# Kernel tuning notes

Hardware: AMD Instinct MI355X
Metric: run time of the kernel (lower is better)

Reference implementation:

```python
import jax, jax.numpy as jnp
import numpy as np

N_NODES = 50000
N_EDGES = 800000
IN_DIM = 128
HIDDEN = 64
HEADS = 4
N_GRAPHS = 256
NEG_SLOPE = 0.2  # PyG GATConv default


def gat_conv(x, src, dst, W, a_src, a_dst, b):
    """PyG-style GATConv (concat=True), eval mode (no dropout).
    x: [N, F_in]; src/dst: [E] (self-loops already included);
    W: [H*C, F_in]; a_src/a_dst: [H, C]; b: [H*C].
    """
    N = x.shape[0]
    H, C = a_src.shape
    h = (x @ W.T).reshape(N, H, C)                      # [N, H, C]
    alo = (h * a_src[None]).sum(-1)                     # [N, H]
    ahi = (h * a_dst[None]).sum(-1)                     # [N, H]
    e = jax.nn.leaky_relu(alo[src] + ahi[dst], NEG_SLOPE)  # [E, H]
    # segment softmax over destination neighborhoods
    m = jax.ops.segment_max(e, dst, num_segments=N)     # [N, H]
    ex = jnp.exp(e - m[dst])
    denom = jax.ops.segment_sum(ex, dst, num_segments=N)
    alpha = ex / (denom[dst] + 1e-16)                   # [E, H]
    out = jax.ops.segment_sum(h[src] * alpha[:, :, None], dst, num_segments=N)
    return out.reshape(N, H * C) + b


def setup_inputs() -> dict:
    key = jax.random.key(0)
    ks = jax.random.split(key, 24)
    p = lambda k, s: (jax.random.normal(k, s, jnp.float32) * 0.1)
    x = jax.random.normal(ks[0], (N_NODES, IN_DIM), jnp.float32)
    edge_index = jax.random.randint(ks[1], (2, N_EDGES), 0, N_NODES, jnp.int64 if jax.config.jax_enable_x64 else jnp.int32)
    batch_idx = jnp.sort(jax.random.randint(ks[2], (N_NODES,), 0, N_GRAPHS))
    HC = HIDDEN * HEADS
    return {
        "x": x, "edge_index": edge_index, "batch_idx": batch_idx,
        "W1": p(ks[3], (HC, IN_DIM)), "as1": p(ks[4], (HEADS, HIDDEN)), "ad1": p(ks[5], (HEADS, HIDDEN)), "b1": jnp.zeros((HC,), jnp.float32),
        "W2": p(ks[6], (HC, HC)), "as2": p(ks[7], (HEADS, HIDDEN)), "ad2": p(ks[8], (HEADS, HIDDEN)), "b2": jnp.zeros((HC,), jnp.float32),
        "W3": p(ks[9], (HIDDEN, HC)), "as3": p(ks[10], (1, HIDDEN)), "ad3": p(ks[11], (1, HIDDEN)), "b3": jnp.zeros((HIDDEN,), jnp.float32),
        "Wc1": p(ks[12], (HIDDEN, HIDDEN)), "bc1": jnp.zeros((HIDDEN,), jnp.float32),
        "Wc2": p(ks[13], (1, HIDDEN)), "bc2": jnp.zeros((1,), jnp.float32),
        "Wr1": p(ks[14], (HIDDEN, HIDDEN)), "br1": jnp.zeros((HIDDEN,), jnp.float32),
        "Wr2": p(ks[15], (1, HIDDEN)), "br2": jnp.zeros((1,), jnp.float32),
    }


def reference(x, edge_index, batch_idx, W1, as1, ad1, b1, W2, as2, ad2, b2, W3, as3, ad3, b3, Wc1, bc1, Wc2, bc2, Wr1, br1, Wr2, br2):
    N = x.shape[0]
    loops = jnp.arange(N, dtype=edge_index.dtype)
    src = jnp.concatenate([edge_index[0], loops])  # add_self_loops=True (PyG default)
    dst = jnp.concatenate([edge_index[1], loops])
    h = jax.nn.elu(gat_conv(x, src, dst, W1, as1, ad1, b1))
    h = jax.nn.elu(gat_conv(h, src, dst, W2, as2, ad2, b2))
    h = jax.nn.elu(gat_conv(h, src, dst, W3, as3, ad3, b3))  # [N, HIDDEN]
    # global mean pool over graphs
    cnt = jax.ops.segment_sum(jnp.ones((N,), h.dtype), batch_idx, num_segments=N_GRAPHS)
    g = jax.ops.segment_sum(h, batch_idx, num_segments=N_GRAPHS) / jnp.maximum(cnt, 1.0)[:, None]
    cls_logit = (jax.nn.relu(g @ Wc1.T + bc1) @ Wc2.T + bc2).reshape(-1)
    reg_pred = (jax.nn.relu(g @ Wr1.T + br1) @ Wr2.T + br2).reshape(-1)
    return (cls_logit, reg_pred)
```

## Files before the change

kernel.cpp:

```cpp
#include <hip/hip_runtime.h>

#define N_NODES 50000
#define N_EDGES 800000
#define EP_EDGES (N_EDGES + N_NODES)
#define N_GRAPHS 256
#define NBLK_SCAN ((N_NODES + 255) / 256)
#define POOL_CHUNK ((N_NODES + 255) / 256)

typedef unsigned short u16;
typedef __attribute__((ext_vector_type(8))) short s8v;
typedef __attribute__((ext_vector_type(4))) float f4v;

__device__ __forceinline__ u16 fb(float f) {
  unsigned u = __float_as_uint(f);
  return (u16)((u + 0x7fffu + ((u >> 16) & 1u)) >> 16);
}
__device__ __forceinline__ float bfl(unsigned p) {
  return __uint_as_float(p << 16);
}
__device__ __forceinline__ float bfh(unsigned p) {
  return __uint_as_float(p & 0xffff0000u);
}
__device__ __forceinline__ float bff(u16 s) {
  return __uint_as_float(((unsigned)s) << 16);
}

#define W_N1 32768
#define W_N2 (W_N1 + 65536)
#define W_N3 (W_N2 + 16384)
__global__ void f2bw(const float* __restrict__ w1, const float* __restrict__ w2,
                     const float* __restrict__ w3, u16* __restrict__ w1b,
                     u16* __restrict__ w2b, u16* __restrict__ w3b) {
  int i = blockIdx.x * 256 + threadIdx.x;
  if (i < W_N1) w1b[i] = fb(w1[i]);
  else if (i < W_N2) w2b[i - W_N1] = fb(w2[i - W_N1]);
  else if (i < W_N3) w3b[i - W_N2] = fb(w3[i - W_N2]);
}

__device__ __forceinline__ void score_epilogue(
    f4v (&acc)[4][4], const float* __restrict__ a_src,
    const float* __restrict__ a_dst, float* __restrict__ alo,
    float* __restrict__ ahi, int m0, int n0, int wi, int wj, int quad, int fr,
    int M) {
  const int head = (n0 + wj) >> 6;
  float as[4], ad[4];
#pragma unroll
  for (int j = 0; j < 4; ++j) {
    int col = n0 + wj + j * 16 + fr;
    as[j] = a_src[col];
    ad[j] = a_dst[col];
  }
#pragma unroll
  for (int i = 0; i < 4; ++i) {
#pragma unroll
    for (int r = 0; r < 4; ++r) {
      float s = 0.f, d = 0.f;
#pragma unroll
      for (int j = 0; j < 4; ++j) {
        s += acc[i][j][r] * as[j];
        d += acc[i][j][r] * ad[j];
      }
#pragma unroll
      for (int off = 8; off; off >>= 1) {
        s += __shfl_xor(s, off, 64);
        d += __shfl_xor(d, off, 64);
      }
      int row = m0 + wi + i * 16 + quad * 4 + r;
      if (fr == 0 && row < M) {
        alo[row * 4 + head] = s;
        ahi[row * 4 + head] = d;
      }
    }
  }
}

__global__ __launch_bounds__(256) void gemm128(
    const u16* __restrict__ A, const u16* __restrict__ W,
    u16* __restrict__ C, const float* __restrict__ a_src,
    const float* __restrict__ a_dst, float* __restrict__ alo,
    float* __restrict__ ahi, int M, int Nout, int K) {
  __shared__ u16 As[128][40];
  __shared__ u16 Bs[128][40];
  const int t = threadIdx.x;
  const int m0 = blockIdx.y * 128, n0 = blockIdx.x * 128;
  const int rq = t >> 2, q = t & 3;
  const int w = t >> 6, lane = t & 63;
  const int wi = (w & 1) * 64, wj = (w >> 1) * 64;
  const int quad = lane >> 4, fr = lane & 15;

  f4v acc[4][4] = {};
  for (int k0 = 0; k0 < K; k0 += 32) {
    uint4 av[2], bv[2];
#pragma unroll
    for (int g = 0; g < 2; ++g) {
      int r = rq + g * 64;
      int m = m0 + r;
      av[g] = (m < M) ? *(const uint4*)&A[(size_t)m * K + k0 + q * 8]
                      : make_uint4(0, 0, 0, 0);
      bv[g] = *(const uint4*)&W[(size_t)(n0 + r) * K + k0 + q * 8];
    }
    __syncthreads();
#pragma unroll
    for (int g = 0; g < 2; ++g) {
      *(uint4*)&As[rq + g * 64][q * 8] = av[g];
      *(uint4*)&Bs[rq + g * 64][q * 8] = bv[g];
    }
    __syncthreads();
    s8v af[4], bf_[4];
#pragma unroll
    for (int i = 0; i < 4; ++i) {
      af[i] = *(const s8v*)&As[wi + i * 16 + fr][quad * 8];
      bf_[i] = *(const s8v*)&Bs[wj + i * 16 + fr][quad * 8];
    }
#pragma unroll
    for (int i = 0; i < 4; ++i)
#pragma unroll
      for (int j = 0; j < 4; ++j)
        acc[i][j] =
            __builtin_amdgcn_mfma_f32_16x16x32_bf16(af[i], bf_[j], acc[i][j], 0, 0, 0);
  }
#pragma unroll
  for (int i = 0; i < 4; ++i) {
    int rbase = m0 + wi + i * 16 + quad * 4;
#pragma unroll
    for (int j = 0; j < 4; ++j) {
      int col = n0 + wj + j * 16 + fr;
#pragma unroll
      for (int r = 0; r < 4; ++r) {
        int row = rbase + r;
        if (row < M) C[(size_t)row * Nout + col] = fb(acc[i][j][r]);
      }
    }
  }
  score_epilogue(acc, a_src, a_dst, alo, ahi, m0, n0, wi, wj, quad, fr, M);
}

__global__ __launch_bounds__(256) void gemm128_f32(
    const float* __restrict__ A, const u16* __restrict__ W,
    u16* __restrict__ C, const float* __restrict__ a_src,
    const float* __restrict__ a_dst, float* __restrict__ alo,
    float* __restrict__ ahi, int M, int Nout, int K) {
  __shared__ u16 As[128][40];
  __shared__ u16 Bs[128][40];
  const int t = threadIdx.x;
  const int m0 = blockIdx.y * 128, n0 = blockIdx.x * 128;
  const int rq = t >> 2, q = t & 3;
  const int w = t >> 6, lane = t & 63;
  const int wi = (w & 1) * 64, wj = (w >> 1) * 64;
  const int quad = lane >> 4, fr = lane & 15;

  f4v acc[4][4] = {};
  for (int k0 = 0; k0 < K; k0 += 32) {
    uint4 av[2], bv[2];
#pragma unroll
    for (int g = 0; g < 2; ++g) {
      int r = rq + g * 64;
      int m = m0 + r;
      if (m < M) {
        float4 f0 = *(const float4*)&A[(size_t)m * K + k0 + q * 8];
        float4 f1 = *(const float4*)&A[(size_t)m * K + k0 + q * 8 + 4];
        av[g].x = (unsigned)fb(f0.x) | ((unsigned)fb(f0.y) << 16);
        av[g].y = (unsigned)fb(f0.z) | ((unsigned)fb(f0.w) << 16);
        av[g].z = (unsigned)fb(f1.x) | ((unsigned)fb(f1.y) << 16);
        av[g].w = (unsigned)fb(f1.z) | ((unsigned)fb(f1.w) << 16);
      } else {
        av[g] = make_uint4(0, 0, 0, 0);
      }
      bv[g] = *(const uint4*)&W[(size_t)(n0 + r) * K + k0 + q * 8];
    }
    __syncthreads();
#pragma unroll
    for (int g = 0; g < 2; ++g) {
      *(uint4*)&As[rq + g * 64][q * 8] = av[g];
      *(uint4*)&Bs[rq + g * 64][q * 8] = bv[g];
    }
    __syncthreads();
    s8v af[4], bf_[4];
#pragma unroll
    for (int i = 0; i < 4; ++i) {
      af[i] = *(const s8v*)&As[wi + i * 16 + fr][quad * 8];
      bf_[i] = *(const s8v*)&Bs[wj + i * 16 + fr][quad * 8];
    }
#pragma unroll
    for (int i = 0; i < 4; ++i)
#pragma unroll
      for (int j = 0; j < 4; ++j)
        acc[i][j] =
            __builtin_amdgcn_mfma_f32_16x16x32_bf16(af[i], bf_[j], acc[i][j], 0, 0, 0);
  }
#pragma unroll
  for (int i = 0; i < 4; ++i) {
    int rbase = m0 + wi + i * 16 + quad * 4;
#pragma unroll
    for (int j = 0; j < 4; ++j) {
      int col = n0 + wj + j * 16 + fr;
#pragma unroll
      for (int r = 0; r < 4; ++r) {
        int row = rbase + r;
        if (row < M) C[(size_t)row * Nout + col] = fb(acc[i][j][r]);
      }
    }
  }
  score_epilogue(acc, a_src, a_dst, alo, ahi, m0, n0, wi, wj, quad, fr, M);
}

__global__ __launch_bounds__(256) void gemm_bf16(
    const u16* __restrict__ A, const u16* __restrict__ W,
    u16* __restrict__ C, int M, int Nout, int K) {
  __shared__ u16 As[64][40];
  __shared__ u16 Bs[64][40];
  const int t = threadIdx.x;
  const int m0 = blockIdx.y * 64, n0 = blockIdx.x * 64;
  const int r = t >> 2, c = t & 3;
  const int w = t >> 6, lane = t & 63;
  const int mi = (w & 1) * 32, ni = (w >> 1) * 32;
  const int quad = lane >> 4, fr = lane & 15;

  f4v c00{}, c01{}, c10{}, c11{};
  for (int k0 = 0; k0 < K; k0 += 32) {
    uint4 av = make_uint4(0, 0, 0, 0);
    int m = m0 + r;
    if (m < M) av = *(const uint4*)&A[(size_t)m * K + k0 + c * 8];
    uint4 bv = *(const uint4*)&W[(size_t)(n0 + r) * K + k0 + c * 8];
    __syncthreads();
    *(uint4*)&As[r][c * 8] = av;
    *(uint4*)&Bs[r][c * 8] = bv;
    __syncthreads();
    s8v a0 = *(const s8v*)&As[mi + fr][quad * 8];
    s8v a1 = *(const s8v*)&As[mi + 16 + fr][quad * 8];
    s8v b0 = *(const s8v*)&Bs[ni + fr][quad * 8];
    s8v b1 = *(const s8v*)&Bs[ni + 16 + fr][quad * 8];
    c00 = __builtin_amdgcn_mfma_f32_16x16x32_bf16(a0, b0, c00, 0, 0, 0);
    c01 = __builtin_amdgcn_mfma_f32_16x16x32_bf16(a0, b1, c01, 0, 0, 0);
    c10 = __builtin_amdgcn_mfma_f32_16x16x32_bf16(a1, b0, c10, 0, 0, 0);
    c11 = __builtin_amdgcn_mfma_f32_16x16x32_bf16(a1, b1, c11, 0, 0, 0);
  }
  const int col = n0 + ni + fr;
#pragma unroll
  for (int i = 0; i < 4; ++i) {
    int row = m0 + mi + quad * 4 + i;
    if (row < M) {
      C[(size_t)row * Nout + col] = fb(c00[i]);
      C[(size_t)row * Nout + col + 16] = fb(c01[i]);
    }
    int row2 = row + 16;
    if (row2 < M) {
      C[(size_t)row2 * Nout + col] = fb(c10[i]);
      C[(size_t)row2 * Nout + col + 16] = fb(c11[i]);
    }
  }
}

__global__ void k_hist(const int* __restrict__ ei, int* __restrict__ deg) {
  int e = blockIdx.x * 256 + threadIdx.x;
  if (e >= EP_EDGES) return;
  int d = (e < N_EDGES) ? ei[N_EDGES + e] : e - N_EDGES;
  atomicAdd(&deg[d], 1);
}

__global__ void k_scan_local(const int* __restrict__ deg,
                             int* __restrict__ rowstart,
                             int* __restrict__ bsum) {
  __shared__ int sh[256];
  const int tid = threadIdx.x;
  const int i = blockIdx.x * 256 + tid;
  int v = (i < N_NODES) ? deg[i] : 0;
  sh[tid] = v;
  __syncthreads();
  for (int off = 1; off < 256; off <<= 1) {
    int add = (tid >= off) ? sh[tid - off] : 0;
    __syncthreads();
    sh[tid] += add;
    __syncthreads();
  }
  if (i < N_NODES) rowstart[i] = sh[tid] - v;
  if (tid == 255) bsum[blockIdx.x] = sh[255];
}

__global__ void k_scan_bsum(int* __restrict__ bsum, int* __restrict__ boff) {
  __shared__ int sh[256];
  const int tid = threadIdx.x;
  int v = (tid < NBLK_SCAN) ? bsum[tid] : 0;
  sh[tid] = v;
  __syncthreads();
  for (int off = 1; off < 256; off <<= 1) {
    int add = (tid >= off) ? sh[tid - off] : 0;
    __syncthreads();
    sh[tid] += add;
    __syncthreads();
  }
  boff[tid] = sh[tid] - v;
}

__global__ void k_scan_add(int* __restrict__ rowstart,
                           const int* __restrict__ boff) {
  int i = blockIdx.x * 256 + threadIdx.x;
  if (i < N_NODES) rowstart[i] += boff[i >> 8];
  if (i == N_NODES) rowstart[N_NODES] = EP_EDGES;
}

__global__ void k_scatter(const int* __restrict__ ei,
                          const int* __restrict__ rowstart,
                          int* __restrict__ fill, int* __restrict__ esrc) {
  int e = blockIdx.x * 256 + threadIdx.x;
  if (e >= EP_EDGES) return;
  int s, d;
  if (e < N_EDGES) { s = ei[e]; d = ei[N_EDGES + e]; }
  else             { s = d = e - N_EDGES; }
  int pos = rowstart[d] + atomicAdd(&fill[d], 1);
  esrc[pos] = s;
}

__global__ __launch_bounds__(256) void attn_scores1(
    const u16* __restrict__ h, const float* __restrict__ a_src,
    const float* __restrict__ a_dst, float* __restrict__ alo,
    float* __restrict__ ahi) {
  const int t = threadIdx.x;
  const int n = blockIdx.x * 4 + (t >> 6);
  const int lane = t & 63;
  float v = bff(h[(size_t)n * 64 + lane]);
  float s = v * a_src[lane];
  float d = v * a_dst[lane];
#pragma unroll
  for (int off = 32; off; off >>= 1) {
    s += __shfl_xor(s, off, 64);
    d += __shfl_xor(d, off, 64);
  }
  if (lane == 0) {
    alo[n] = s;
    ahi[n] = d;
  }
}

__global__ __launch_bounds__(64) void agg3_4(
    const int* __restrict__ rowstart, const int* __restrict__ esrc,
    const u16* __restrict__ hbuf, const float* __restrict__ alo,
    const float* __restrict__ ahi, const float* __restrict__ bias,
    u16* __restrict__ feat) {
  const int d = blockIdx.x;
  const int lane = threadIdx.x;
  const int head = lane >> 4;
  const int l16 = lane & 15;
  const int c = lane * 4;
  const int s0 = rowstart[d], s1 = rowstart[d + 1];
  const float ah = ahi[d * 4 + head];

  float sm = 0.f;
  for (int j = s0 + l16; j < s1; j += 16) {
    int s = esrc[j];
    float e = alo[s * 4 + head] + ah;
    e = e > 0.f ? e : 0.2f * e;
    sm += __expf(e);
  }
#pragma unroll
  for (int off = 8; off; off >>= 1) sm += __shfl_xor(sm, off, 64);
  const float linv = 1.f / (sm + 1e-16f);

  float o0 = 0.f, o1 = 0.f, o2 = 0.f, o3 = 0.f;
  for (int j = s0; j < s1; j += 8) {
    int ss[8];
    float wq[8];
#pragma unroll
    for (int q = 0; q < 8; ++q) {
      int jj = j + q;
      int sv = esrc[jj < EP_EDGES ? jj : EP_EDGES - 1];
      ss[q] = (jj < s1) ? sv : d;
    }
#pragma unroll
    for (int q = 0; q < 8; ++q) {
      float e = alo[ss[q] * 4 + head] + ah;
      e = e > 0.f ? e : 0.2f * e;
      wq[q] = (j + q < s1) ? __expf(e) * linv : 0.f;
    }
    uint2 hv[8];
#pragma unroll
    for (int q = 0; q < 8; ++q)
      hv[q] = *(const uint2*)&hbuf[(size_t)ss[q] * 256 + c];
#pragma unroll
    for (int q = 0; q < 8; ++q) {
      o0 += wq[q] * bfl(hv[q].x);
      o1 += wq[q] * bfh(hv[q].x);
      o2 += wq[q] * bfl(hv[q].y);
      o3 += wq[q] * bfh(hv[q].y);
    }
  }
  float4 bv = *(const float4*)&bias[c];
  float v0 = o0 + bv.x, v1 = o1 + bv.y, v2 = o2 + bv.z, v3 = o3 + bv.w;
  v0 = v0 > 0.f ? v0 : __expf(v0) - 1.f;
  v1 = v1 > 0.f ? v1 : __expf(v1) - 1.f;
  v2 = v2 > 0.f ? v2 : __expf(v2) - 1.f;
  v3 = v3 > 0.f ? v3 : __expf(v3) - 1.f;
  uint2 pv;
  pv.x = (unsigned)fb(v0) | ((unsigned)fb(v1) << 16);
  pv.y = (unsigned)fb(v2) | ((unsigned)fb(v3) << 16);
  *(uint2*)&feat[(size_t)d * 256 + c] = pv;
}

__global__ __launch_bounds__(64) void agg3_1(
    const int* __restrict__ rowstart, const int* __restrict__ esrc,
    const u16* __restrict__ hbuf, const float* __restrict__ alo,
    const float* __restrict__ ahi, const float* __restrict__ bias,
    float* __restrict__ feat) {
  const int d = blockIdx.x;
  const int t = threadIdx.x;
  const int s0 = rowstart[d], s1 = rowstart[d + 1];
  const float ah = ahi[d];

  float sm = 0.f;
  for (int j = s0 + t; j < s1; j += 64) {
    int s = esrc[j];
    float e = alo[s] + ah;
    e = e > 0.f ? e : 0.2f * e;
    sm += __expf(e);
  }
#pragma unroll
  for (int off = 32; off; off >>= 1) sm += __shfl_xor(sm, off, 64);
  const float linv = 1.f / (sm + 1e-16f);

  float o = 0.f;
  for (int j = s0; j < s1; j += 8) {
    int ss[8];
    float wq[8];
#pragma unroll
    for (int q = 0; q < 8; ++q) {
      int jj = j + q;
      int sv = esrc[jj < EP_EDGES ? jj : EP_EDGES - 1];
      ss[q] = (jj < s1) ? sv : d;
    }
#pragma unroll
    for (int q = 0; q < 8; ++q) {
      float e = alo[ss[q]] + ah;
      e = e > 0.f ? e : 0.2f * e;
      wq[q] = (j + q < s1) ? __expf(e) * linv : 0.f;
    }
    u16 hv[8];
#pragma unroll
    for (int q = 0; q < 8; ++q) hv[q] = hbuf[(size_t)ss[q] * 64 + t];
#pragma unroll
    for (int q = 0; q < 8; ++q) o += wq[q] * bff(hv[q]);
  }
  float v = o + bias[t];
  feat[(size_t)d * 64 + t] = v > 0.f ? v : __expf(v) - 1.f;
}

__global__ __launch_bounds__(64) void pool_seg(
    const float* __restrict__ feat, const int* __restrict__ batch,
    float* __restrict__ gsum, float* __restrict__ gcnt) {
  const int b = blockIdx.x;
  const int t = threadIdx.x;
  int n0 = b * POOL_CHUNK;
  int n1 = n0 + POOL_CHUNK;
  if (n1 > N_NODES) n1 = N_NODES;
  if (n0 >= n1) return;
  int g = batch[n0];
  float acc = 0.f;
  int cnt = 0;
  for (int n = n0; n < n1; ++n) {
    int gn = batch[n];
    if (gn != g) {
      atomicAdd(&gsum[g * 64 + t], acc);
      if (t == 0) atomicAdd(&gcnt[g], (float)cnt);
      acc = 0.f; cnt = 0; g = gn;
    }
    acc += feat[(size_t)n * 64 + t];
    ++cnt;
  }
  atomicAdd(&gsum[g * 64 + t], acc);
  if (t == 0) atomicAdd(&gcnt[g], (float)cnt);
}

__global__ void heads(const float* __restrict__ gsum,
                      const float* __restrict__ gcnt,
                      const float* __restrict__ Wc1, const float* __restrict__ bc1,
                      const float* __restrict__ Wc2, const float* __restrict__ bc2,
                      const float* __restrict__ Wr1, const float* __restrict__ br1,
                      const float* __restrict__ Wr2, const float* __restrict__ br2,
                      float* __restrict__ out) {
  __shared__ float g[64];
  const int gi = blockIdx.x, j = threadIdx.x;
  float cnt = gcnt[gi];
  cnt = cnt < 1.f ? 1.f : cnt;
  g[j] = gsum[gi * 64 + j] / cnt;
  __syncthreads();
  float hc = bc1[j], hr = br1[j];
#pragma unroll 8
  for (int c = 0; c < 64; ++c) {
    float gv = g[c];
    hc += gv * Wc1[j * 64 + c];
    hr += gv * Wr1[j * 64 + c];
  }
  hc = fmaxf(hc, 0.f) * Wc2[j];
  hr = fmaxf(hr, 0.f) * Wr2[j];
#pragma unroll
  for (int off = 32; off; off >>= 1) {
    hc += __shfl_down(hc, off, 64);
    hr += __shfl_down(hr, off, 64);
  }
  if (j == 0) {
    out[gi] = hc + bc2[0];
    out[N_GRAPHS + gi] = hr + br2[0];
  }
}

extern "C" void kernel_launch(void* const* d_in, const int* in_sizes, int n_in,
                              void* d_out, int out_size, void* d_ws,
                              size_t ws_size, hipStream_t stream) {
  const float* x   = (const float*)d_in[0];
  const int* ei    = (const int*)d_in[1];
  const int* batch = (const int*)d_in[2];
  const float* W1  = (const float*)d_in[3];
  const float* as1 = (const float*)d_in[4];
  const float* ad1 = (const float*)d_in[5];
  const float* b1  = (const float*)d_in[6];
  const float* W2  = (const float*)d_in[7];
  const float* as2 = (const float*)d_in[8];
  const float* ad2 = (const float*)d_in[9];
  const float* b2  = (const float*)d_in[10];
  const float* W3  = (const float*)d_in[11];
  const float* as3 = (const float*)d_in[12];
  const float* ad3 = (const float*)d_in[13];
  const float* b3  = (const float*)d_in[14];
  const float* Wc1 = (const float*)d_in[15];
  const float* bc1 = (const float*)d_in[16];
  const float* Wc2 = (const float*)d_in[17];
  const float* bc2 = (const float*)d_in[18];
  const float* Wr1 = (const float*)d_in[19];
  const float* br1 = (const float*)d_in[20];
  const float* Wr2 = (const float*)d_in[21];
  const float* br2 = (const float*)d_in[22];
  float* out = (float*)d_out;

  float* ws = (float*)d_ws;
  u16* h_buf = (u16*)ws;
  float* p = ws + (size_t)N_NODES * 128;
  u16* featb = (u16*)p;
  p += (size_t)N_NODES * 128;
  u16* W1b = (u16*)p; p += 16384;
  u16* W2b = (u16*)p; p += 32768;
  u16* W3b = (u16*)p; p += 8192;
  float* feat3 = p;   p += (size_t)N_NODES * 64;
  float* alo   = p;   p += (size_t)N_NODES * 4;
  float* ahi   = p;   p += (size_t)N_NODES * 4;
  int* rowstart = (int*)p; p += (N_NODES + 4);
  int* esrc    = (int*)p;  p += EP_EDGES;
  float* gsum  = p;   p += N_GRAPHS * 64;
  float* gcnt  = p;
  int* deg  = (int*)alo;
  int* fill = (int*)alo + N_NODES;
  int* bsum = (int*)gsum;
  int* boff = (int*)gsum + 256;

  hipMemsetAsync(deg, 0, (size_t)2 * N_NODES * 4, stream);
  const int eblk = (EP_EDGES + 255) / 256;
  k_hist<<<eblk, 256, 0, stream>>>(ei, deg);
  k_scan_local<<<NBLK_SCAN, 256, 0, stream>>>(deg, rowstart, bsum);
  k_scan_bsum<<<1, 256, 0, stream>>>(bsum, boff);
  k_scan_add<<<(N_NODES + 256) / 256, 256, 0, stream>>>(rowstart, boff);
  k_scatter<<<eblk, 256, 0, stream>>>(ei, rowstart, fill, esrc);

  f2bw<<<(W_N3 + 255) / 256, 256, 0, stream>>>(W1, W2, W3, W1b, W2b, W3b);

  const int MB128 = (N_NODES + 127) / 128;
  const int MB64 = (N_NODES + 63) / 64;
  gemm128_f32<<<dim3(2, MB128), 256, 0, stream>>>(x, W1b, h_buf, as1, ad1, alo,
                                                  ahi, N_NODES, 256, 128);
  agg3_4<<<N_NODES, 64, 0, stream>>>(rowstart, esrc, h_buf, alo, ahi, b1,
                                     featb);
  gemm128<<<dim3(2, MB128), 256, 0, stream>>>(featb, W2b, h_buf, as2, ad2, alo,
                                              ahi, N_NODES, 256, 256);
  agg3_4<<<N_NODES, 64, 0, stream>>>(rowstart, esrc, h_buf, alo, ahi, b2,
                                     featb);
  gemm_bf16<<<dim3(1, MB64), 256, 0, stream>>>(featb, W3b, h_buf, N_NODES, 64, 256);
  attn_scores1<<<N_NODES / 4, 256, 0, stream>>>(h_buf, as3, ad3, alo, ahi);
  agg3_1<<<N_NODES, 64, 0, stream>>>(rowstart, esrc, h_buf, alo, ahi, b3,
                                     feat3);

  hipMemsetAsync(gsum, 0, (size_t)(N_GRAPHS * 64 + N_GRAPHS) * 4, stream);
  pool_seg<<<N_GRAPHS, 64, 0, stream>>>(feat3, batch, gsum, gcnt);
  heads<<<N_GRAPHS, 64, 0, stream>>>(gsum, gcnt, Wc1, bc1, Wc2, bc2, Wr1, br1,
                                     Wr2, br2, out);
}
```

Before: 558.7 us.

## Fuse softmax denominator into aggregation and merge pooling with MLP heads

```diff
diff --git a/kernel.cpp b/kernel.cpp
--- a/kernel.cpp
+++ b/kernel.cpp
@@ -5,7 +5,6 @@
 #define EP_EDGES (N_EDGES + N_NODES)
 #define N_GRAPHS 256
 #define NBLK_SCAN ((N_NODES + 255) / 256)
-#define POOL_CHUNK ((N_NODES + 255) / 256)
 
 typedef unsigned short u16;
 typedef __attribute__((ext_vector_type(8))) short s8v;
@@ -311,28 +310,7 @@
   esrc[pos] = s;
 }
 
-__global__ __launch_bounds__(256) void attn_scores1(
-    const u16* __restrict__ h, const float* __restrict__ a_src,
-    const float* __restrict__ a_dst, float* __restrict__ alo,
-    float* __restrict__ ahi) {
-  const int t = threadIdx.x;
-  const int n = blockIdx.x * 4 + (t >> 6);
-  const int lane = t & 63;
-  float v = bff(h[(size_t)n * 64 + lane]);
-  float s = v * a_src[lane];
-  float d = v * a_dst[lane];
-#pragma unroll
-  for (int off = 32; off; off >>= 1) {
-    s += __shfl_xor(s, off, 64);
-    d += __shfl_xor(d, off, 64);
-  }
-  if (lane == 0) {
-    alo[n] = s;
-    ahi[n] = d;
-  }
-}
-
-__global__ __launch_bounds__(64) void agg3_4(
+__global__ __launch_bounds__(64) void agg4(
     const int* __restrict__ rowstart, const int* __restrict__ esrc,
     const u16* __restrict__ hbuf, const float* __restrict__ alo,
     const float* __restrict__ ahi, const float* __restrict__ bias,
@@ -340,23 +318,11 @@
   const int d = blockIdx.x;
   const int lane = threadIdx.x;
   const int head = lane >> 4;
-  const int l16 = lane & 15;
   const int c = lane * 4;
   const int s0 = rowstart[d], s1 = rowstart[d + 1];
   const float ah = ahi[d * 4 + head];
 
-  float sm = 0.f;
-  for (int j = s0 + l16; j < s1; j += 16) {
-    int s = esrc[j];
-    float e = alo[s * 4 + head] + ah;
-    e = e > 0.f ? e : 0.2f * e;
-    sm += __expf(e);
-  }
-#pragma unroll
-  for (int off = 8; off; off >>= 1) sm += __shfl_xor(sm, off, 64);
-  const float linv = 1.f / (sm + 1e-16f);
-
-  float o0 = 0.f, o1 = 0.f, o2 = 0.f, o3 = 0.f;
+  float l = 0.f, o0 = 0.f, o1 = 0.f, o2 = 0.f, o3 = 0.f;
   for (int j = s0; j < s1; j += 8) {
     int ss[8];
     float wq[8];
@@ -370,7 +336,7 @@
     for (int q = 0; q < 8; ++q) {
       float e = alo[ss[q] * 4 + head] + ah;
       e = e > 0.f ? e : 0.2f * e;
-      wq[q] = (j + q < s1) ? __expf(e) * linv : 0.f;
+      wq[q] = (j + q < s1) ? __expf(e) : 0.f;
     }
     uint2 hv[8];
 #pragma unroll
@@ -378,14 +344,17 @@
       hv[q] = *(const uint2*)&hbuf[(size_t)ss[q] * 256 + c];
 #pragma unroll
     for (int q = 0; q < 8; ++q) {
+      l += wq[q];
       o0 += wq[q] * bfl(hv[q].x);
       o1 += wq[q] * bfh(hv[q].x);
       o2 += wq[q] * bfl(hv[q].y);
       o3 += wq[q] * bfh(hv[q].y);
     }
   }
+  const float inv = 1.f / (l + 1e-16f);
   float4 bv = *(const float4*)&bias[c];
-  float v0 = o0 + bv.x, v1 = o1 + bv.y, v2 = o2 + bv.z, v3 = o3 + bv.w;
+  float v0 = o0 * inv + bv.x, v1 = o1 * inv + bv.y;
+  float v2 = o2 * inv + bv.z, v3 = o3 * inv + bv.w;
   v0 = v0 > 0.f ? v0 : __expf(v0) - 1.f;
   v1 = v1 > 0.f ? v1 : __expf(v1) - 1.f;
   v2 = v2 > 0.f ? v2 : __expf(v2) - 1.f;
@@ -396,107 +365,88 @@
   *(uint2*)&feat[(size_t)d * 256 + c] = pv;
 }
 
-__global__ __launch_bounds__(64) void agg3_1(
+__global__ __launch_bounds__(64) void agg1(
     const int* __restrict__ rowstart, const int* __restrict__ esrc,
-    const u16* __restrict__ hbuf, const float* __restrict__ alo,
-    const float* __restrict__ ahi, const float* __restrict__ bias,
+    const u16* __restrict__ hbuf, const float* __restrict__ a_src,
+    const float* __restrict__ a_dst, const float* __restrict__ bias,
     float* __restrict__ feat) {
   const int d = blockIdx.x;
   const int t = threadIdx.x;
   const int s0 = rowstart[d], s1 = rowstart[d + 1];
-  const float ah = ahi[d];
-
-  float sm = 0.f;
-  for (int j = s0 + t; j < s1; j += 64) {
-    int s = esrc[j];
-    float e = alo[s] + ah;
-    e = e > 0.f ? e : 0.2f * e;
-    sm += __expf(e);
-  }
-#pragma unroll
-  for (int off = 32; off; off >>= 1) sm += __shfl_xor(sm, off, 64);
-  const float linv = 1.f / (sm + 1e-16f);
-
-  float o = 0.f;
-  for (int j = s0; j < s1; j += 8) {
-    int ss[8];
-    float wq[8];
-#pragma unroll
-    for (int q = 0; q < 8; ++q) {
+  const float as = a_src[t];
+
+  float hd = bff(hbuf[(size_t)d * 64 + t]);
+  float ah = hd * a_dst[t];
+#pragma unroll
+  for (int off = 32; off; off >>= 1) ah += __shfl_xor(ah, off, 64);
+
+  float l = 0.f, o = 0.f;
+  for (int j = s0; j < s1; j += 4) {
+    int ss[4];
+    u16 hv[4];
+#pragma unroll
+    for (int q = 0; q < 4; ++q) {
       int jj = j + q;
       int sv = esrc[jj < EP_EDGES ? jj : EP_EDGES - 1];
       ss[q] = (jj < s1) ? sv : d;
     }
 #pragma unroll
-    for (int q = 0; q < 8; ++q) {
-      float e = alo[ss[q]] + ah;
+    for (int q = 0; q < 4; ++q) hv[q] = hbuf[(size_t)ss[q] * 64 + t];
+#pragma unroll
+    for (int q = 0; q < 4; ++q) {
+      float hq = bff(hv[q]);
+      float al = hq * as;
+#pragma unroll
+      for (int off = 32; off; off >>= 1) al += __shfl_xor(al, off, 64);
+      float e = al + ah;
       e = e > 0.f ? e : 0.2f * e;
-      wq[q] = (j + q < s1) ? __expf(e) * linv : 0.f;
-    }
-    u16 hv[8];
-#pragma unroll
-    for (int q = 0; q < 8; ++q) hv[q] = hbuf[(size_t)ss[q] * 64 + t];
-#pragma unroll
-    for (int q = 0; q < 8; ++q) o += wq[q] * bff(hv[q]);
-  }
-  float v = o + bias[t];
+      float w = (j + q < s1) ? __expf(e) : 0.f;
+      l += w;
+      o += w * hq;
+    }
+  }
+  float v = o / (l + 1e-16f) + bias[t];
   feat[(size_t)d * 64 + t] = v > 0.f ? v : __expf(v) - 1.f;
 }
 
-__global__ __launch_bounds__(64) void pool_seg(
+__global__ __launch_bounds__(64) void poolheads(
     const float* __restrict__ feat, const int* __restrict__ batch,
-    float* __restrict__ gsum, float* __restrict__ gcnt) {
-  const int b = blockIdx.x;
-  const int t = threadIdx.x;
-  int n0 = b * POOL_CHUNK;
-  int n1 = n0 + POOL_CHUNK;
-  if (n1 > N_NODES) n1 = N_NODES;
-  if (n0 >= n1) return;
-  int g = batch[n0];
+    const float* __restrict__ Wc1, const float* __restrict__ bc1,
+    const float* __restrict__ Wc2, const float* __restrict__ bc2,
+    const float* __restrict__ Wr1, const float* __restrict__ br1,
+    const float* __restrict__ Wr2, const float* __restrict__ br2,
+    float* __restrict__ out) {
+  const int gi = blockIdx.x, t = threadIdx.x;
+  int l = 0, r = N_NODES;
+  while (l < r) { int m = (l + r) >> 1; if (batch[m] < gi) l = m + 1; else r = m; }
+  const int lo = l;
+  r = N_NODES;
+  while (l < r) { int m = (l + r) >> 1; if (batch[m] < gi + 1) l = m + 1; else r = m; }
+  const int hi = l;
+
   float acc = 0.f;
-  int cnt = 0;
-  for (int n = n0; n < n1; ++n) {
-    int gn = batch[n];
-    if (gn != g) {
-      atomicAdd(&gsum[g * 64 + t], acc);
-      if (t == 0) atomicAdd(&gcnt[g], (float)cnt);
-      acc = 0.f; cnt = 0; g = gn;
-    }
-    acc += feat[(size_t)n * 64 + t];
-    ++cnt;
-  }
-  atomicAdd(&gsum[g * 64 + t], acc);
-  if (t == 0) atomicAdd(&gcnt[g], (float)cnt);
-}
-
-__global__ void heads(const float* __restrict__ gsum,
-                      const float* __restrict__ gcnt,
-                      const float* __restrict__ Wc1, const float* __restrict__ bc1,
-                      const float* __restrict__ Wc2, const float* __restrict__ bc2,
-                      const float* __restrict__ Wr1, const float* __restrict__ br1,
-                      const float* __restrict__ Wr2, const float* __restrict__ br2,
-                      float* __restrict__ out) {
+  for (int n = lo; n < hi; ++n) acc += feat[(size_t)n * 64 + t];
+  float cnt = (float)(hi - lo);
+  cnt = cnt < 1.f ? 1.f : cnt;
+
   __shared__ float g[64];
-  const int gi = blockIdx.x, j = threadIdx.x;
-  float cnt = gcnt[gi];
-  cnt = cnt < 1.f ? 1.f : cnt;
-  g[j] = gsum[gi * 64 + j] / cnt;
+  g[t] = acc / cnt;
   __syncthreads();
-  float hc = bc1[j], hr = br1[j];
+  float hc = bc1[t], hr = br1[t];
 #pragma unroll 8
   for (int c = 0; c < 64; ++c) {
     float gv = g[c];
-    hc += gv * Wc1[j * 64 + c];
-    hr += gv * Wr1[j * 64 + c];
-  }
-  hc = fmaxf(hc, 0.f) * Wc2[j];
-  hr = fmaxf(hr, 0.f) * Wr2[j];
+    hc += gv * Wc1[t * 64 + c];
+    hr += gv * Wr1[t * 64 + c];
+  }
+  hc = fmaxf(hc, 0.f) * Wc2[t];
+  hr = fmaxf(hr, 0.f) * Wr2[t];
 #pragma unroll
   for (int off = 32; off; off >>= 1) {
     hc += __shfl_down(hc, off, 64);
     hr += __shfl_down(hr, off, 64);
   }
-  if (j == 0) {
+  if (t == 0) {
     out[gi] = hc + bc2[0];
     out[N_GRAPHS + gi] = hr + br2[0];
   }
@@ -543,12 +493,11 @@
   float* ahi   = p;   p += (size_t)N_NODES * 4;
   int* rowstart = (int*)p; p += (N_NODES + 4);
   int* esrc    = (int*)p;  p += EP_EDGES;
-  float* gsum  = p;   p += N_GRAPHS * 64;
-  float* gcnt  = p;
+  float* bsc   = p;
   int* deg  = (int*)alo;
   int* fill = (int*)alo + N_NODES;
-  int* bsum = (int*)gsum;
-  int* boff = (int*)gsum + 256;
+  int* bsum = (int*)bsc;
+  int* boff = (int*)bsc + 256;
 
   hipMemsetAsync(deg, 0, (size_t)2 * N_NODES * 4, stream);
   const int eblk = (EP_EDGES + 255) / 256;
@@ -564,19 +513,13 @@
   const int MB64 = (N_NODES + 63) / 64;
   gemm128_f32<<<dim3(2, MB128), 256, 0, stream>>>(x, W1b, h_buf, as1, ad1, alo,
                                                   ahi, N_NODES, 256, 128);
-  agg3_4<<<N_NODES, 64, 0, stream>>>(rowstart, esrc, h_buf, alo, ahi, b1,
-                                     featb);
+  agg4<<<N_NODES, 64, 0, stream>>>(rowstart, esrc, h_buf, alo, ahi, b1, featb);
   gemm128<<<dim3(2, MB128), 256, 0, stream>>>(featb, W2b, h_buf, as2, ad2, alo,
                                               ahi, N_NODES, 256, 256);
-  agg3_4<<<N_NODES, 64, 0, stream>>>(rowstart, esrc, h_buf, alo, ahi, b2,
-                                     featb);
+  agg4<<<N_NODES, 64, 0, stream>>>(rowstart, esrc, h_buf, alo, ahi, b2, featb);
   gemm_bf16<<<dim3(1, MB64), 256, 0, stream>>>(featb, W3b, h_buf, N_NODES, 64, 256);
-  attn_scores1<<<N_NODES / 4, 256, 0, stream>>>(h_buf, as3, ad3, alo, ahi);
-  agg3_1<<<N_NODES, 64, 0, stream>>>(rowstart, esrc, h_buf, alo, ahi, b3,
-                                     feat3);
-
-  hipMemsetAsync(gsum, 0, (size_t)(N_GRAPHS * 64 + N_GRAPHS) * 4, stream);
-  pool_seg<<<N_GRAPHS, 64, 0, stream>>>(feat3, batch, gsum, gcnt);
-  heads<<<N_GRAPHS, 64, 0, stream>>>(gsum, gcnt, Wc1, bc1, Wc2, bc2, Wr1, br1,
-                                     Wr2, br2, out);
-}
+  agg1<<<N_NODES, 64, 0, stream>>>(rowstart, esrc, h_buf, as3, ad3, b3, feat3);
+
+  poolheads<<<N_GRAPHS, 64, 0, stream>>>(feat3, batch, Wc1, bc1, Wc2, bc2, Wr1,
+                                         br1, Wr2, br2, out);
+}
```

Result: no change. 561.8 us (+0.6%).
